# Kernel optimization log

Measured on AMD Instinct MI355X. Metric: run time of the kernel, lower is better.

## Reference

```python
import jax, jax.numpy as jnp
import numpy as np

TEMPERATURE = 0.1


def setup_inputs() -> dict:
    key = jax.random.key(0)
    features = jax.random.normal(key, (512, 256, 256), dtype=jnp.float32)
    return {"features": features}


def reference(features) -> jnp.ndarray:
    # features: [B, T, D]
    B, T, D = features.shape
    eps = 1e-12  # torch F.normalize default eps
    f = features / jnp.maximum(
        jnp.linalg.norm(features, axis=-1, keepdims=True), eps
    )  # [B, T, D] L2-normalized
    # Full similarity matrix: one batched matmul instead of T-1 small einsums.
    sim = jnp.einsum("bqd,btd->bqt", f, f) / TEMPERATURE  # [B, T, T]
    logits = sim[:, : T - 1, :]  # anchors t = 0..T-2, [B, T-1, T]
    # Cross-entropy with label t+1 for anchor t:
    # CE = logsumexp(logits) - logits[label]
    lse = jax.nn.logsumexp(logits, axis=-1)  # [B, T-1]
    idx = jnp.arange(T - 1)
    target_logit = logits[:, idx, idx + 1]  # [B, T-1]
    # Original: for each t, mean over B, then sum over t, then / (T-1)
    # == mean over both B and t dims.
    return jnp.mean(lse - target_logit)
```

## Files before the change

kernel.cpp:

```cpp
#include <hip/hip_runtime.h>


typedef float f32x4  __attribute__((ext_vector_type(4)));
typedef float f32x16 __attribute__((ext_vector_type(16)));
typedef unsigned int u32x2 __attribute__((ext_vector_type(2)));
typedef unsigned int u32x4 __attribute__((ext_vector_type(4)));
typedef __bf16 bf16x8 __attribute__((ext_vector_type(8)));

#define NB 512
#define NT 256
#define ND 256
#define K10L2E 14.42695041f

#define MFMA32 __builtin_amdgcn_mfma_f32_32x32x16_bf16

__device__ __forceinline__ unsigned int f2bf_rne(float f) {
  unsigned int u = __float_as_uint(f);
  return (u + 0x7fffu + ((u >> 16) & 1u)) >> 16;
}

__device__ __forceinline__ void wg_barrier() {
  asm volatile("s_waitcnt lgkmcnt(0)" ::: "memory");
  __builtin_amdgcn_s_barrier();
  asm volatile("" ::: "memory");
}

__device__ __forceinline__ u32x2 pack_bf16x4(f32x4 v) {
  u32x2 o;
  o.x = f2bf_rne(v.x) | (f2bf_rne(v.y) << 16);
  o.y = f2bf_rne(v.z) | (f2bf_rne(v.w) << 16);
  return o;
}

__global__ __launch_bounds__(1024, 4) void fused_kernel(
    const float* __restrict__ x, float* __restrict__ partial) {
  __shared__ u32x4 ck[2][128 * 8];
  __shared__ float invbuf[NT];
  __shared__ float sbuf[NT][5];
  __shared__ float tbuf[NT];
  __shared__ float redbuf[16];

  const int t    = threadIdx.x;
  const int wave = t >> 6;
  const int lane = t & 63;
  const int lo5  = lane & 31;
  const int hi   = lane >> 5;
  const int sxd  = (lo5 >> 1) & 7;
  const int sx4  = (lo5 & 1) * 4;

  const int tr = wave >> 2;
  const int tc = wave & 3;
  const int R = tr * 64, C = tc * 64;

  const int iA = ((R + lo5) >> 1) * 8;
  const int iB = ((C + lo5) >> 1) * 8;

  const int srow = wave * 16;
  const int rrow = srow + (lane >> 2);
  const int qa   = lane & 3;

#define ISSUE(SET, TC) do {                                                  \
    const float* bp = x + ((size_t)blockIdx.x + (size_t)((TC) >> 3) * 256)   \
                          * (NT * ND) + ((TC) & 7) * 32;                     \
    SET[0] = *(const f32x4*)(bp + rrow * ND + qa * 4);                       \
    SET[1] = *(const f32x4*)(bp + rrow * ND + (qa + 4) * 4);                 \
  } while (0)

#define CAST_WRITE(BUF, SET) do {                                            \
    _Pragma("unroll")                                                        \
    for (int i = 0; i < 2; ++i) {                                            \
      const int c = qa + i * 4;                                              \
      const u32x2 o = pack_bf16x4(SET[i]);                                   \
      const int s = c >> 1, half = c & 1;                                    \
      const int slot16 = ((rrow & 1) * 4 + s) ^ ((rrow >> 1) & 7);           \
      *(u32x2*)((unsigned int*)&ck[BUF][0]                                   \
                + ((rrow >> 1) * 32 + slot16 * 4 + half * 2)) = o;           \
    }                                                                        \
  } while (0)

#define MFMA_CHUNK(BUF) do {                                                 \
    const u32x4* cb = &ck[BUF][0];                                           \
    _Pragma("unroll")                                                        \
    for (int kb = 0; kb < 2; ++kb) {                                         \
      const int ko = (sx4 + kb * 2 + hi) ^ sxd;                              \
      bf16x8 fa0 = __builtin_bit_cast(bf16x8, cb[iA + ko]);                  \
      bf16x8 fa1 = __builtin_bit_cast(bf16x8, cb[iA + 128 + ko]);            \
      bf16x8 fb0 = __builtin_bit_cast(bf16x8, cb[iB + ko]);                  \
      bf16x8 fb1 = __builtin_bit_cast(bf16x8, cb[iB + 128 + ko]);            \
      a0 = MFMA32(fa0, fb0, a0, 0, 0, 0);                                    \
      a1 = MFMA32(fa0, fb1, a1, 0, 0, 0);                                    \
      a2 = MFMA32(fa1, fb0, a2, 0, 0, 0);                                    \
      a3 = MFMA32(fa1, fb1, a3, 0, 0, 0);                                    \
    }                                                                        \
  } while (0)

  f32x16 a0, a1, a2, a3;
#pragma unroll
  for (int e = 0; e < 16; ++e) { a0[e] = 0.f; a1[e] = 0.f; a2[e] = 0.f; a3[e] = 0.f; }

  f32x4 ldA[2], ldB[2];
  ISSUE(ldA, 0);
  ISSUE(ldB, 1);

#pragma unroll 1
  for (int g = 0; g < 16; g += 2) {
    CAST_WRITE(0, ldA);
    if (g + 2 < 16) ISSUE(ldA, g + 2);
    wg_barrier();
    MFMA_CHUNK(0);

    CAST_WRITE(1, ldB);
    if (g + 3 < 16) ISSUE(ldB, g + 3);
    wg_barrier();
    MFMA_CHUNK(1);

    if (((g + 1) & 7) == 7) {
      const int bb = (int)blockIdx.x + ((g + 1) >> 3) * 256;

      if (tr == tc) {
        float dv0 = 1.0f, dv1 = 1.0f;
#pragma unroll
        for (int rg = 0; rg < 16; ++rg) {
          const int rowe = (rg & 3) + 8 * (rg >> 2) + 4 * hi;
          if (rowe == lo5) { dv0 = a0[rg]; dv1 = a3[rg]; }
        }
        if (hi == ((lo5 >> 2) & 1)) {
          invbuf[R + lo5]      = rsqrtf(fmaxf(dv0, 1e-24f));
          invbuf[R + 32 + lo5] = rsqrtf(fmaxf(dv1, 1e-24f));
        }
      }
      wg_barrier();

      {
        const float ic0 = invbuf[C + lo5] * K10L2E;
        const float ic1 = invbuf[C + 32 + lo5] * K10L2E;
        float e0 = 0.f, e1 = 0.f;
#pragma unroll
        for (int rg = 0; rg < 16; ++rg) {
          const int rowe = (rg & 3) + 8 * (rg >> 2) + 4 * hi;
          const float ir0 = invbuf[R + rowe], ir1 = invbuf[R + 32 + rowe];
          e0 += exp2f(fmaf(a0[rg] * ir0, ic0, -K10L2E));
          e0 += exp2f(fmaf(a2[rg] * ir1, ic0, -K10L2E));
          e1 += exp2f(fmaf(a1[rg] * ir0, ic1, -K10L2E));
          e1 += exp2f(fmaf(a3[rg] * ir1, ic1, -K10L2E));
        }
        e0 += __shfl_xor(e0, 32);
        e1 += __shfl_xor(e1, 32);
        if (hi == 0) sbuf[C + lo5][tr] = e0;
        else         sbuf[C + 32 + lo5][tr] = e1;
      }

      if (tc == tr || tc == tr + 1) {
#pragma unroll
        for (int ar = 0; ar < 2; ++ar) {
#pragma unroll
          for (int rg = 0; rg < 16; ++rg) {
            const int r = R + ar * 32 + (rg & 3) + 8 * (rg >> 2) + 4 * hi;
            const int tcol = r + 1 - C;
            if (r < NT - 1 && tcol >= 0 && tcol < 64 && lo5 == (tcol & 31)) {
              const float v = (tcol < 32) ? (ar ? a2[rg] : a0[rg])
                                          : (ar ? a3[rg] : a1[rg]);
              tbuf[r] = 10.0f * v * invbuf[r] * invbuf[r + 1];
            }
          }
        }
      }
      wg_barrier();

      float val = 0.0f;
      if (t < NT - 1) {
        const float s = sbuf[t][0] + sbuf[t][1] + sbuf[t][2] + sbuf[t][3];
        val = 10.0f + __logf(s) - tbuf[t];
      }
#pragma unroll
      for (int dd = 1; dd < 64; dd <<= 1) val += __shfl_xor(val, dd);
      if (lane == 0) redbuf[wave] = val;
      wg_barrier();
      if (t == 0) {
        float s = 0.f;
#pragma unroll
        for (int w = 0; w < 16; ++w) s += redbuf[w];
        partial[bb] = s;
      }

#pragma unroll
      for (int e = 0; e < 16; ++e) { a0[e] = 0.f; a1[e] = 0.f; a2[e] = 0.f; a3[e] = 0.f; }
    }
  }
#undef ISSUE
#undef CAST_WRITE
#undef MFMA_CHUNK
}

__global__ __launch_bounds__(256) void reduce_kernel(
    const float* __restrict__ partial, float* __restrict__ out) {
  const int t = threadIdx.x;
  float v = partial[t] + partial[t + 256];
#pragma unroll
  for (int d = 1; d < 64; d <<= 1) v += __shfl_xor(v, d);
  __shared__ float red[4];
  if ((t & 63) == 0) red[t >> 6] = v;
  __syncthreads();
  if (t == 0)
    out[0] = (red[0] + red[1] + red[2] + red[3]) * (1.0f / (float)(NB * (NT - 1)));
}

extern "C" void kernel_launch(void* const* d_in, const int* in_sizes, int n_in,
                              void* d_out, int out_size, void* d_ws, size_t ws_size,
                              hipStream_t stream) {
  (void)in_sizes; (void)n_in; (void)out_size; (void)ws_size;
  const float* x = (const float*)d_in[0];
  float* out = (float*)d_out;
  float* partial = (float*)d_ws;

  hipLaunchKernelGGL(fused_kernel, dim3(NB / 2), dim3(1024), 0, stream, x, partial);
  hipLaunchKernelGGL(reduce_kernel, dim3(1), dim3(256), 0, stream, partial, out);
}
```

Measured before the change: 41.85 us.

## Load whole batch tile into LDS once instead of double-buffered K-chunk pipeline

Replaces the double-buffered 32-column K-chunk pipeline, which needed two barriers per chunk, with a single bulk load per batch item. Each item's full 256x256 tile is converted to bf16 and stored in a 128KB swizzled LDS buffer, then all 16 MFMA k-steps run without intermediate barriers. This cuts barrier count and issues larger, fully coalesced global loads (16 per thread in flight). The cost is that global loads no longer overlap with MFMA compute inside a block, the larger LDS footprint may limit occupancy to one block per CU, and the 16 f32x4 load registers per thread add register pressure.

```diff
diff --git a/kernel.cpp b/kernel.cpp
--- a/kernel.cpp
+++ b/kernel.cpp
@@ -19,22 +19,9 @@
   return (u + 0x7fffu + ((u >> 16) & 1u)) >> 16;
 }
 
-__device__ __forceinline__ void wg_barrier() {
-  asm volatile("s_waitcnt lgkmcnt(0)" ::: "memory");
-  __builtin_amdgcn_s_barrier();
-  asm volatile("" ::: "memory");
-}
-
-__device__ __forceinline__ u32x2 pack_bf16x4(f32x4 v) {
-  u32x2 o;
-  o.x = f2bf_rne(v.x) | (f2bf_rne(v.y) << 16);
-  o.y = f2bf_rne(v.z) | (f2bf_rne(v.w) << 16);
-  return o;
-}
-
 __global__ __launch_bounds__(1024, 4) void fused_kernel(
     const float* __restrict__ x, float* __restrict__ partial) {
-  __shared__ u32x4 ck[2][128 * 8];
+  __shared__ u32x4 X[NT * 32];
   __shared__ float invbuf[NT];
   __shared__ float sbuf[NT][5];
   __shared__ float tbuf[NT];
@@ -45,151 +32,122 @@
   const int lane = t & 63;
   const int lo5  = lane & 31;
   const int hi   = lane >> 5;
-  const int sxd  = (lo5 >> 1) & 7;
-  const int sx4  = (lo5 & 1) * 4;
+  const int sx6  = lo5 & 6;
+  const int hx   = hi ^ (lo5 & 1);
 
   const int tr = wave >> 2;
   const int tc = wave & 3;
   const int R = tr * 64, C = tc * 64;
-
-  const int iA = ((R + lo5) >> 1) * 8;
-  const int iB = ((C + lo5) >> 1) * 8;
-
-  const int srow = wave * 16;
-  const int rrow = srow + (lane >> 2);
-  const int qa   = lane & 3;
-
-#define ISSUE(SET, TC) do {                                                  \
-    const float* bp = x + ((size_t)blockIdx.x + (size_t)((TC) >> 3) * 256)   \
-                          * (NT * ND) + ((TC) & 7) * 32;                     \
-    SET[0] = *(const f32x4*)(bp + rrow * ND + qa * 4);                       \
-    SET[1] = *(const f32x4*)(bp + rrow * ND + (qa + 4) * 4);                 \
-  } while (0)
-
-#define CAST_WRITE(BUF, SET) do {                                            \
-    _Pragma("unroll")                                                        \
-    for (int i = 0; i < 2; ++i) {                                            \
-      const int c = qa + i * 4;                                              \
-      const u32x2 o = pack_bf16x4(SET[i]);                                   \
-      const int s = c >> 1, half = c & 1;                                    \
-      const int slot16 = ((rrow & 1) * 4 + s) ^ ((rrow >> 1) & 7);           \
-      *(u32x2*)((unsigned int*)&ck[BUF][0]                                   \
-                + ((rrow >> 1) * 32 + slot16 * 4 + half * 2)) = o;           \
-    }                                                                        \
-  } while (0)
-
-#define MFMA_CHUNK(BUF) do {                                                 \
-    const u32x4* cb = &ck[BUF][0];                                           \
-    _Pragma("unroll")                                                        \
-    for (int kb = 0; kb < 2; ++kb) {                                         \
-      const int ko = (sx4 + kb * 2 + hi) ^ sxd;                              \
-      bf16x8 fa0 = __builtin_bit_cast(bf16x8, cb[iA + ko]);                  \
-      bf16x8 fa1 = __builtin_bit_cast(bf16x8, cb[iA + 128 + ko]);            \
-      bf16x8 fb0 = __builtin_bit_cast(bf16x8, cb[iB + ko]);                  \
-      bf16x8 fb1 = __builtin_bit_cast(bf16x8, cb[iB + 128 + ko]);            \
-      a0 = MFMA32(fa0, fb0, a0, 0, 0, 0);                                    \
-      a1 = MFMA32(fa0, fb1, a1, 0, 0, 0);                                    \
-      a2 = MFMA32(fa1, fb0, a2, 0, 0, 0);                                    \
-      a3 = MFMA32(fa1, fb1, a3, 0, 0, 0);                                    \
-    }                                                                        \
-  } while (0)
-
-  f32x16 a0, a1, a2, a3;
-#pragma unroll
-  for (int e = 0; e < 16; ++e) { a0[e] = 0.f; a1[e] = 0.f; a2[e] = 0.f; a3[e] = 0.f; }
-
-  f32x4 ldA[2], ldB[2];
-  ISSUE(ldA, 0);
-  ISSUE(ldB, 1);
+  const int iA0 = (R + lo5) * 32;
+  const int iA1 = (R + 32 + lo5) * 32;
+  const int iB0 = (C + lo5) * 32;
+  const int iB1 = (C + 32 + lo5) * 32;
 
 #pragma unroll 1
-  for (int g = 0; g < 16; g += 2) {
-    CAST_WRITE(0, ldA);
-    if (g + 2 < 16) ISSUE(ldA, g + 2);
-    wg_barrier();
-    MFMA_CHUNK(0);
+  for (int b = 0; b < 2; ++b) {
+    const float* xb = x + ((size_t)blockIdx.x + (size_t)b * 256) * (NT * ND);
 
-    CAST_WRITE(1, ldB);
-    if (g + 3 < 16) ISSUE(ldB, g + 3);
-    wg_barrier();
-    MFMA_CHUNK(1);
+    {
+      f32x4 ld[16];
+#pragma unroll
+      for (int i = 0; i < 16; ++i)
+        ld[i] = *(const f32x4*)(xb + (wave * 16 + i) * ND + lane * 4);
+#pragma unroll
+      for (int i = 0; i < 16; ++i) {
+        const int r = wave * 16 + i;
+        u32x2 o;
+        o.x = f2bf_rne(ld[i].x) | (f2bf_rne(ld[i].y) << 16);
+        o.y = f2bf_rne(ld[i].z) | (f2bf_rne(ld[i].w) << 16);
+        const int slot = (lane >> 1) ^ (r & 7);
+        *(u32x2*)((unsigned int*)X + (r * 128 + slot * 4 + (lane & 1) * 2)) = o;
+      }
+    }
+    __syncthreads();
 
-    if (((g + 1) & 7) == 7) {
-      const int bb = (int)blockIdx.x + ((g + 1) >> 3) * 256;
+    f32x16 a0, a1, a2, a3;
+#pragma unroll
+    for (int e = 0; e < 16; ++e) { a0[e] = 0.f; a1[e] = 0.f; a2[e] = 0.f; a3[e] = 0.f; }
 
-      if (tr == tc) {
-        float dv0 = 1.0f, dv1 = 1.0f;
+#pragma unroll 4
+    for (int kb = 0; kb < 16; ++kb) {
+      const int ko = ((kb * 2) ^ sx6) | hx;
+      bf16x8 fa0 = __builtin_bit_cast(bf16x8, X[iA0 + ko]);
+      bf16x8 fa1 = __builtin_bit_cast(bf16x8, X[iA1 + ko]);
+      bf16x8 fb0 = __builtin_bit_cast(bf16x8, X[iB0 + ko]);
+      bf16x8 fb1 = __builtin_bit_cast(bf16x8, X[iB1 + ko]);
+      a0 = MFMA32(fa0, fb0, a0, 0, 0, 0);
+      a1 = MFMA32(fa0, fb1, a1, 0, 0, 0);
+      a2 = MFMA32(fa1, fb0, a2, 0, 0, 0);
+      a3 = MFMA32(fa1, fb1, a3, 0, 0, 0);
+    }
+
+    if (tr == tc) {
+      float dv0 = 1.0f, dv1 = 1.0f;
+#pragma unroll
+      for (int rg = 0; rg < 16; ++rg) {
+        const int rowe = (rg & 3) + 8 * (rg >> 2) + 4 * hi;
+        if (rowe == lo5) { dv0 = a0[rg]; dv1 = a3[rg]; }
+      }
+      if (hi == ((lo5 >> 2) & 1)) {
+        invbuf[R + lo5]      = rsqrtf(fmaxf(dv0, 1e-24f));
+        invbuf[R + 32 + lo5] = rsqrtf(fmaxf(dv1, 1e-24f));
+      }
+    }
+    __syncthreads();
+
+    {
+      const float ic0 = invbuf[C + lo5] * K10L2E;
+      const float ic1 = invbuf[C + 32 + lo5] * K10L2E;
+      float e0 = 0.f, e1 = 0.f;
+#pragma unroll
+      for (int rg = 0; rg < 16; ++rg) {
+        const int rowe = (rg & 3) + 8 * (rg >> 2) + 4 * hi;
+        const float ir0 = invbuf[R + rowe], ir1 = invbuf[R + 32 + rowe];
+        e0 += exp2f(fmaf(a0[rg] * ir0, ic0, -K10L2E));
+        e0 += exp2f(fmaf(a2[rg] * ir1, ic0, -K10L2E));
+        e1 += exp2f(fmaf(a1[rg] * ir0, ic1, -K10L2E));
+        e1 += exp2f(fmaf(a3[rg] * ir1, ic1, -K10L2E));
+      }
+      e0 += __shfl_xor(e0, 32);
+      e1 += __shfl_xor(e1, 32);
+      if (hi == 0) sbuf[C + lo5][tr] = e0;
+      else         sbuf[C + 32 + lo5][tr] = e1;
+    }
+
+    if (tc == tr || tc == tr + 1) {
+#pragma unroll
+      for (int ar = 0; ar < 2; ++ar) {
 #pragma unroll
         for (int rg = 0; rg < 16; ++rg) {
-          const int rowe = (rg & 3) + 8 * (rg >> 2) + 4 * hi;
-          if (rowe == lo5) { dv0 = a0[rg]; dv1 = a3[rg]; }
-        }
-        if (hi == ((lo5 >> 2) & 1)) {
-          invbuf[R + lo5]      = rsqrtf(fmaxf(dv0, 1e-24f));
-          invbuf[R + 32 + lo5] = rsqrtf(fmaxf(dv1, 1e-24f));
-        }
-      }
-      wg_barrier();
-
-      {
-        const float ic0 = invbuf[C + lo5] * K10L2E;
-        const float ic1 = invbuf[C + 32 + lo5] * K10L2E;
-        float e0 = 0.f, e1 = 0.f;
-#pragma unroll
-        for (int rg = 0; rg < 16; ++rg) {
-          const int rowe = (rg & 3) + 8 * (rg >> 2) + 4 * hi;
-          const float ir0 = invbuf[R + rowe], ir1 = invbuf[R + 32 + rowe];
-          e0 += exp2f(fmaf(a0[rg] * ir0, ic0, -K10L2E));
-          e0 += exp2f(fmaf(a2[rg] * ir1, ic0, -K10L2E));
-          e1 += exp2f(fmaf(a1[rg] * ir0, ic1, -K10L2E));
-          e1 += exp2f(fmaf(a3[rg] * ir1, ic1, -K10L2E));
-        }
-        e0 += __shfl_xor(e0, 32);
-        e1 += __shfl_xor(e1, 32);
-        if (hi == 0) sbuf[C + lo5][tr] = e0;
-        else         sbuf[C + 32 + lo5][tr] = e1;
-      }
-
-      if (tc == tr || tc == tr + 1) {
-#pragma unroll
-        for (int ar = 0; ar < 2; ++ar) {
-#pragma unroll
-          for (int rg = 0; rg < 16; ++rg) {
-            const int r = R + ar * 32 + (rg & 3) + 8 * (rg >> 2) + 4 * hi;
-            const int tcol = r + 1 - C;
-            if (r < NT - 1 && tcol >= 0 && tcol < 64 && lo5 == (tcol & 31)) {
-              const float v = (tcol < 32) ? (ar ? a2[rg] : a0[rg])
-                                          : (ar ? a3[rg] : a1[rg]);
-              tbuf[r] = 10.0f * v * invbuf[r] * invbuf[r + 1];
-            }
+          const int r = R + ar * 32 + (rg & 3) + 8 * (rg >> 2) + 4 * hi;
+          const int tcol = r + 1 - C;
+          if (r < NT - 1 && tcol >= 0 && tcol < 64 && lo5 == (tcol & 31)) {
+            const float v = (tcol < 32) ? (ar ? a2[rg] : a0[rg])
+                                        : (ar ? a3[rg] : a1[rg]);
+            tbuf[r] = 10.0f * v * invbuf[r] * invbuf[r + 1];
           }
         }
       }
-      wg_barrier();
+    }
+    __syncthreads();
 
-      float val = 0.0f;
-      if (t < NT - 1) {
-        const float s = sbuf[t][0] + sbuf[t][1] + sbuf[t][2] + sbuf[t][3];
-        val = 10.0f + __logf(s) - tbuf[t];
-      }
+    float val = 0.0f;
+    if (t < NT - 1) {
+      const float s = sbuf[t][0] + sbuf[t][1] + sbuf[t][2] + sbuf[t][3];
+      val = 10.0f + __logf(s) - tbuf[t];
+    }
 #pragma unroll
-      for (int dd = 1; dd < 64; dd <<= 1) val += __shfl_xor(val, dd);
-      if (lane == 0) redbuf[wave] = val;
-      wg_barrier();
-      if (t == 0) {
-        float s = 0.f;
+    for (int dd = 1; dd < 64; dd <<= 1) val += __shfl_xor(val, dd);
+    if (lane == 0) redbuf[wave] = val;
+    __syncthreads();
+    if (t == 0) {
+      float s = 0.f;
 #pragma unroll
-        for (int w = 0; w < 16; ++w) s += redbuf[w];
-        partial[bb] = s;
-      }
-
-#pragma unroll
-      for (int e = 0; e < 16; ++e) { a0[e] = 0.f; a1[e] = 0.f; a2[e] = 0.f; a3[e] = 0.f; }
+      for (int w = 0; w < 16; ++w) s += redbuf[w];
+      partial[blockIdx.x + b * 256] = s;
     }
+    __syncthreads();
   }
-#undef ISSUE
-#undef CAST_WRITE
-#undef MFMA_CHUNK
 }
 
 __global__ __launch_bounds__(256) void reduce_kernel(
```

Measured after the change: 48.72 us. 16.4% more time.
